# Optimization experiments

Hardware: AMD Instinct MI355X
Metric: run time of the kernel (lower is better)

## Reference

```python
import jax, jax.numpy as jnp
import numpy as np

DIM = 48
HEADS = 8
DIM1 = DIM * HEADS  # 384
RED = 16


def setup_inputs() -> dict:
    key = jax.random.key(0)
    ks = jax.random.split(key, 10)
    s = 0.02
    return {
        "x": jax.random.normal(ks[0], (4, DIM, 128, 128), dtype=jnp.float32),
        "qkv_w": jax.random.normal(ks[1], (DIM1 * 4, DIM), dtype=jnp.float32) * s,
        "dw_w": jax.random.normal(ks[2], (DIM1 * 4, HEADS, 3, 3), dtype=jnp.float32) * s,  # groups=DIM*4 -> 8 in-ch per group
        "po1_w": jax.random.normal(ks[3], (DIM, DIM1), dtype=jnp.float32) * s,
        "fc1_w": jax.random.normal(ks[4], (DIM1 // RED, DIM1), dtype=jnp.float32) * s,
        "fc1_b": jnp.zeros((DIM1 // RED,), dtype=jnp.float32),
        "fc2_w": jax.random.normal(ks[5], (DIM1, DIM1 // RED), dtype=jnp.float32) * s,
        "fc2_b": jnp.zeros((DIM1,), dtype=jnp.float32),
        "temperature": jnp.ones((HEADS, 1, 1), dtype=jnp.float32),
    }


def reference(x, qkv_w, dw_w, po1_w, fc1_w, fc1_b, fc2_w, fc2_b, temperature):
    b, c, h, w = x.shape  # c == dim
    heads = temperature.shape[0]
    # 1x1 pointwise conv: dim -> dim1*4
    qkv = jnp.einsum('bchw,oc->bohw', x, qkv_w)
    # grouped 3x3 conv, groups = dim*4 (8 channels per group)
    qkv = jax.lax.conv_general_dilated(
        qkv, dw_w, window_strides=(1, 1), padding='SAME',
        feature_group_count=c * 4,
        dimension_numbers=('NCHW', 'OIHW', 'NCHW'))
    q, k, v, l = jnp.split(qkv, 4, axis=1)  # each (b, dim1, h, w)
    hw = h * w
    q = q.reshape(b, heads, c, hw)
    k = k.reshape(b, heads, c, hw)
    v = v.reshape(b, heads, c, hw)
    # ChannelAttention on l: note it returns fc2_out * sigmoid(fc2_out)
    avg = jnp.mean(l, axis=(2, 3))  # (b, dim1)
    y = jax.nn.relu(avg @ fc1_w.T + fc1_b)
    y = y @ fc2_w.T + fc2_b  # (b, dim1)
    L = (y * jax.nn.sigmoid(y))[:, :, None, None]  # (b, dim1, 1, 1)
    # L2-normalize over spatial (last) axis, torch eps=1e-12
    q = q / jnp.clip(jnp.linalg.norm(q, axis=-1, keepdims=True), 1e-12)
    k = k / jnp.clip(jnp.linalg.norm(k, axis=-1, keepdims=True), 1e-12)
    # channel-wise attention: (b, heads, c, c)
    attn = jnp.einsum('bhcn,bhdn->bhcd', q, k) * temperature
    attn = jax.nn.softmax(attn, axis=-1)
    out = jnp.einsum('bhcd,bhdn->bhcn', attn, v).reshape(b, heads * c, h, w)
    out = L + out
    out = jnp.einsum('bchw,oc->bohw', out, po1_w) + x
    return out
```

## Files before the change

kernel.cpp:

```cpp
#include <hip/hip_runtime.h>
#include <cstdint>

#define BB 4
#define CC 48
#define HW 16384
#define D1 384
#define HEADS 8

typedef unsigned short ushort_t;
typedef __attribute__((ext_vector_type(8))) short short8;
typedef __attribute__((ext_vector_type(4))) float f32x4;

__device__ __forceinline__ float bf2f(ushort_t u){
  union{uint32_t i; float f;} v; v.i = ((uint32_t)u)<<16; return v.f;
}
__device__ __forceinline__ ushort_t f2bf(float f){
  union{float f; uint32_t i;} v; v.f=f;
  uint32_t x = v.i;
  uint32_t r = (x + 0x7fff + ((x>>16)&1)) >> 16;
  return (ushort_t)r;
}

__global__ __launch_bounds__(256) void k_wf(const float* __restrict__ dw,
                                            const float* __restrict__ qw,
                                            ushort_t* __restrict__ wfp,
                                            float* __restrict__ qn2){
  int oc = blockIdx.x, tid = threadIdx.x;
  if(oc < 19){ int i = oc*256 + tid; if(i < 4800) qn2[i] = 0.f; }
  for(int kk=tid; kk<448; kk+=256){
    int t = kk/48, c = kk - t*48;
    float s = 0.f;
    if(t < 9){
      #pragma unroll
      for(int j=0;j<8;j++)
        s += dw[(size_t)oc*72 + j*9 + t] * qw[(size_t)((oc>>3)*8 + j)*48 + c];
    }
    wfp[(size_t)oc*448 + kk] = f2bf(s);
  }
}

__global__ __launch_bounds__(256) void k_xpose(const float* __restrict__ x,
                                               ushort_t* __restrict__ xb16,
                                               float* __restrict__ xst){
  int gy = blockIdx.x;
  int b  = blockIdx.y;
  ushort_t* orow = xb16 + ((size_t)b*130 + gy)*130*48;
  int tid = threadIdx.x;
  if(gy==0 || gy==129){
    short8 z = {0,0,0,0,0,0,0,0};
    for(int u=tid; u<780; u+=256) *(short8*)(orow + u*8) = z;
    return;
  }
  __shared__ float xl[48*128];
  const float* xr = x + (size_t)b*CC*HW + (size_t)(gy-1)*128;
  for(int i=tid;i<6144;i+=256){
    int c=i>>7, p=i&127;
    xl[c*128+p] = xr[(size_t)c*HW + p];
  }
  __syncthreads();
  for(int u=tid; u<780; u+=256){
    int gx = u/6, s = u-gx*6;
    ushort_t tmp[8];
    if(gx==0||gx==129){
      #pragma unroll
      for(int j=0;j<8;j++) tmp[j]=0;
    } else {
      #pragma unroll
      for(int j=0;j<8;j++) tmp[j] = f2bf(xl[(s*8+j)*128 + (gx-1)]);
    }
    *(short8*)(orow + (size_t)u*8) = *(short8*)tmp;
  }
  if(tid < 48){
    const float* row = &xl[tid*128];
    float a0=0,a1=0,a2=0,a3=0;
    #pragma unroll 8
    for(int p=0;p<128;p+=4){ a0+=row[p]; a1+=row[p+1]; a2+=row[p+2]; a3+=row[p+3]; }
    float s = (a0+a1)+(a2+a3);
    float* o = xst + ((size_t)b*48 + tid)*9;
    atomicAdd(&o[0], s);
    atomicAdd(&o[3], row[0]);
    atomicAdd(&o[4], row[127]);
    if(gy==1)  { o[1]=s; o[5]=row[0]; o[6]=row[127]; }
    if(gy==128){ o[2]=s; o[7]=row[0]; o[8]=row[127]; }
  }
}

#define HROWC 64
__global__ __launch_bounds__(256,3) void k_conv(const ushort_t* __restrict__ xb16,
                                                const ushort_t* __restrict__ wfp,
                                                ushort_t* __restrict__ qkvd){
  __shared__ __align__(16) ushort_t xs[180*HROWC];
  int tid  = threadIdx.x;
  int wave = tid>>6, lane = tid&63;
  int quad = lane>>4, mrow = lane&15;
  int mhalf = wave>>1, nhalf = wave&1;
  int tile = blockIdx.x;
  int ty0 = (tile>>3)*8, tx0 = (tile&7)*16;
  int ocb = blockIdx.y*128 + mhalf*64;
  int b   = blockIdx.z;

  const ushort_t* xh = xb16 + ((size_t)b*16900 + (size_t)ty0*130 + tx0)*48;
  for(int u=tid; u<1944; u+=256){
    int r = u/6, g = u - r*6;
    int hy = r/18, hx = r - hy*18;
    short8 v = *(const short8*)(xh + ((size_t)hy*130 + hx)*48 + g*8);
    *(short8*)(xs + r*HROWC + ((g ^ (r&7))<<3)) = v;
  }
  __syncthreads();

  int rb[4];
  #pragma unroll
  for(int nt=0;nt<4;nt++) rb[nt] = (nhalf*4+nt+1)*18 + mrow + 1;

  const ushort_t* Abase = wfp + (size_t)(ocb + mrow)*448 + quad*8;
  f32x4 Cacc[4][4];
  #pragma unroll
  for(int mt=0;mt<4;mt++)
    #pragma unroll
    for(int nt=0;nt<4;nt++) Cacc[mt][nt] = (f32x4){0.f,0.f,0.f,0.f};

  short8 Ac[4], An[4];
  #pragma unroll
  for(int mt=0;mt<4;mt++) Ac[mt] = *(const short8*)(Abase + (size_t)mt*16*448);

  #pragma unroll
  for(int chunk=0; chunk<14; chunk++){
    if(chunk < 13){
      #pragma unroll
      for(int mt=0;mt<4;mt++)
        An[mt] = *(const short8*)(Abase + (size_t)mt*16*448 + (chunk+1)*32);
    }
    int kq = chunk*32 + quad*8;
    int t  = kq/48;
    int c  = kq - t*48;
    int tc = (t<9) ? t : 8;
    int dyq = tc/3;
    int drow = dyq*18 + (tc - dyq*3) - 19;
    int g = c>>3;
    short8 Bf[4];
    #pragma unroll
    for(int nt=0;nt<4;nt++){
      int r = rb[nt] + drow;
      Bf[nt] = *(const short8*)(xs + r*HROWC + ((g ^ (r&7))<<3));
    }
    #pragma unroll
    for(int mt=0;mt<4;mt++)
      #pragma unroll
      for(int nt=0;nt<4;nt++)
        Cacc[mt][nt] = __builtin_amdgcn_mfma_f32_16x16x32_bf16(Ac[mt], Bf[nt], Cacc[mt][nt], 0,0,0);
    #pragma unroll
    for(int mt=0;mt<4;mt++) Ac[mt] = An[mt];
  }

  #pragma unroll
  for(int mt=0;mt<4;mt++){
    #pragma unroll
    for(int nt=0;nt<4;nt++){
      int py = nhalf*4 + nt;
      int gpos = (ty0+py)*128 + tx0 + mrow;
      #pragma unroll
      for(int r=0;r<4;r++){
        int oc = ocb + mt*16 + quad*4 + r;
        qkvd[((size_t)b*1152 + oc)*HW + gpos] = f2bf(Cacc[mt][nt][r]);
      }
    }
  }
}

__global__ __launch_bounds__(256,3) void k_S(const ushort_t* __restrict__ qkvd,
                                             float* __restrict__ Spart,
                                             float* __restrict__ qn2){
  __shared__ __align__(16) ushort_t qk[96*264];
  int tid = threadIdx.x;
  int blk = blockIdx.x, h = blockIdx.y, b = blockIdx.z;
  int wave = tid>>6, lane = tid&63;
  int quad = lane>>4, mrow = lane&15;
  const ushort_t* qb = qkvd + ((size_t)b*1152 + h*48)*HW;
  const ushort_t* kb = qb + (size_t)384*HW;

  f32x4 accS[3][3], accq[3], acck[3];
  #pragma unroll
  for(int mt=0;mt<3;mt++){
    accq[mt] = (f32x4){0.f,0.f,0.f,0.f};
    acck[mt] = (f32x4){0.f,0.f,0.f,0.f};
    #pragma unroll
    for(int nt=0;nt<3;nt++) accS[mt][nt] = (f32x4){0.f,0.f,0.f,0.f};
  }

  for(int half=0; half<2; half++){
    int p0 = blk*512 + half*256;
    __syncthreads();
    for(int u=tid; u<3072; u+=256){
      int ch = u>>5, px = u&31;
      const ushort_t* src = ((ch<48) ? qb + (size_t)ch*HW
                                     : kb + (size_t)(ch-48)*HW) + p0 + px*8;
      *(short8*)(qk + ch*264 + px*8) = *(const short8*)src;
    }
    __syncthreads();
    #pragma unroll
    for(int ks=0; ks<2; ks++){
      int koff = wave*64 + ks*32 + quad*8;
      short8 Aq[3], Bk[3];
      #pragma unroll
      for(int mt=0;mt<3;mt++) Aq[mt] = *(const short8*)(qk + (mt*16+mrow)*264 + koff);
      #pragma unroll
      for(int nt=0;nt<3;nt++) Bk[nt] = *(const short8*)(qk + (48+nt*16+mrow)*264 + koff);
      #pragma unroll
      for(int mt=0;mt<3;mt++){
        accq[mt] = __builtin_amdgcn_mfma_f32_16x16x32_bf16(Aq[mt], Aq[mt], accq[mt], 0,0,0);
        acck[mt] = __builtin_amdgcn_mfma_f32_16x16x32_bf16(Bk[mt], Bk[mt], acck[mt], 0,0,0);
        #pragma unroll
        for(int nt=0;nt<3;nt++)
          accS[mt][nt] = __builtin_amdgcn_mfma_f32_16x16x32_bf16(Aq[mt], Bk[nt], accS[mt][nt], 0,0,0);
      }
    }
  }
  __syncthreads();
  float* scr = (float*)qk;
  #pragma unroll
  for(int mt=0;mt<3;mt++)
    #pragma unroll
    for(int nt=0;nt<3;nt++)
      #pragma unroll
      for(int r=0;r<4;r++)
        scr[wave*2304 + (mt*16+quad*4+r)*48 + nt*16 + mrow] = accS[mt][nt][r];
  __syncthreads();
  float* outp = Spart + ((size_t)((b*HEADS+h)*32 + blk))*2304;
  for(int idx=tid; idx<2304; idx+=256)
    outp[idx] = scr[idx] + scr[2304+idx] + scr[4608+idx] + scr[6912+idx];
  int rr = mrow - (quad<<2);
  #pragma unroll
  for(int r=0;r<4;r++){
    if(rr == r){
      #pragma unroll
      for(int mt=0;mt<3;mt++){
        atomicAdd(qn2 + (size_t)b*D1 + h*48 + mt*16 + mrow, accq[mt][r]);
        atomicAdd(qn2 + 1536 + (size_t)b*D1 + h*48 + mt*16 + mrow, acck[mt][r]);
      }
    }
  }
}

__global__ __launch_bounds__(384) void k_mlp(const float* __restrict__ xst,
                                             const float* __restrict__ qw,
                                             const float* __restrict__ dw,
                                             const float* __restrict__ fc1w,
                                             const float* __restrict__ fc1b,
                                             const float* __restrict__ fc2w,
                                             const float* __restrict__ fc2b,
                                             const float* __restrict__ po1,
                                             float* __restrict__ constv){
  int b = blockIdx.x, tid = threadIdx.x;
  __shared__ float xsl[432];
  __shared__ float lst[3456];
  __shared__ float avg[384];
  __shared__ float y1[24];
  __shared__ float Lb[384];
  for(int i=tid;i<432;i+=384) xsl[i] = xst[(size_t)b*432 + i];
  __syncthreads();
  {
    float st[9];
    #pragma unroll
    for(int s=0;s<9;s++) st[s]=0.f;
    const float* w = qw + (size_t)(1152+tid)*48;
    for(int c=0;c<48;c++){
      float wv = w[c];
      #pragma unroll
      for(int s=0;s<9;s++) st[s] += wv*xsl[c*9+s];
    }
    #pragma unroll
    for(int s=0;s<9;s++) lst[tid*9+s] = st[s];
  }
  __syncthreads();
  {
    int base = tid & ~7;
    const float* ls = &lst[base*9];
    float s = 0.f;
    #pragma unroll
    for(int i=0;i<8;i++){
      float T=ls[i*9+0],R0=ls[i*9+1],R1=ls[i*9+2],C0=ls[i*9+3],C1=ls[i*9+4];
      float c00=ls[i*9+5],c0W=ls[i*9+6],cH0=ls[i*9+7],cHW=ls[i*9+8];
      const float* wp = dw + (size_t)(1152+tid)*72 + i*9;
      #pragma unroll
      for(int dy=0;dy<3;dy++){
        float rm = (dy==0)?R1:((dy==2)?R0:0.f);
        #pragma unroll
        for(int dx=0;dx<3;dx++){
          float cm = (dx==0)?C1:((dx==2)?C0:0.f);
          float corner = 0.f;
          if(dy==0&&dx==0)corner=cHW;
          if(dy==0&&dx==2)corner=cH0;
          if(dy==2&&dx==0)corner=c0W;
          if(dy==2&&dx==2)corner=c00;
          s += wp[dy*3+dx]*(T-rm-cm+corner);
        }
      }
    }
    avg[tid] = s*(1.f/16384.f);
  }
  __syncthreads();
  if(tid<24){
    float s = fc1b[tid];
    const float* w = fc1w + (size_t)tid*384;
    for(int c=0;c<384;c++) s += w[c]*avg[c];
    y1[tid] = fmaxf(s,0.f);
  }
  __syncthreads();
  {
    float s = fc2b[tid];
    const float* w = fc2w + (size_t)tid*24;
    #pragma unroll
    for(int j=0;j<24;j++) s += w[j]*y1[j];
    Lb[tid] = s/(1.f+__expf(-s));
  }
  __syncthreads();
  if(tid<48){
    const float* w = po1 + (size_t)tid*384;
    float s = 0.f;
    for(int c=0;c<384;c++) s += w[c]*Lb[c];
    constv[b*48+tid] = s;
  }
}

__global__ __launch_bounds__(256) void k_attn(const float* __restrict__ Spart,
                                              const float* __restrict__ qn2,
                                              const float* __restrict__ temp,
                                              const float* __restrict__ po1,
                                              ushort_t* __restrict__ m2o){
  int h = blockIdx.x, b = blockIdx.y, tid = threadIdx.x;
  __shared__ float att[2304];
  __shared__ float nq[48], nk[48];
  const float* kn2 = qn2 + 1536;
  if(tid<48)      nq[tid]    = fmaxf(sqrtf(qn2[(size_t)b*D1 + h*48 + tid]),    1e-12f);
  else if(tid<96) nk[tid-48] = fmaxf(sqrtf(kn2[(size_t)b*D1 + h*48 + tid-48]), 1e-12f);
  __syncthreads();
  float tmp = temp[h];
  const float* Sp = Spart + ((size_t)(b*HEADS+h)*32)*2304;
  for(int idx=tid; idx<2304; idx+=256){
    float s = 0.f;
    for(int blk=0;blk<32;blk++) s += Sp[(size_t)blk*2304 + idx];
    int c = idx/48, d = idx - c*48;
    att[idx] = s*tmp/(nq[c]*nk[d]);
  }
  __syncthreads();
  if(tid<48){
    float* row = &att[tid*48];
    float m = -1e30f;
    for(int d=0;d<48;d++) m = fmaxf(m,row[d]);
    float s = 0.f;
    for(int d=0;d<48;d++){ float e=__expf(row[d]-m); row[d]=e; s+=e; }
    float inv = 1.f/s;
    for(int d=0;d<48;d++) row[d]*=inv;
  }
  __syncthreads();
  for(int idx=tid; idx<2304; idx+=256){
    int d = idx/48, o = idx - d*48;
    float s = 0.f;
    for(int c=0;c<48;c++) s += po1[(size_t)o*D1 + h*48 + c]*att[c*48+d];
    m2o[((size_t)b*48 + o)*D1 + h*48 + d] = f2bf(s);
  }
}

#define FROW2 40
__global__ __launch_bounds__(256,3) void k_final(const ushort_t* __restrict__ qkvd,
                                                 const ushort_t* __restrict__ m2o,
                                                 const float* __restrict__ constv,
                                                 const float* __restrict__ x,
                                                 float* __restrict__ out){
  __shared__ __align__(16) ushort_t vT[2][128*FROW2];
  int tid = threadIdx.x;
  int wave = tid>>6, lane = tid&63;
  int quad = lane>>4, mrow = lane&15;
  int pos0 = blockIdx.x*128;
  int b = blockIdx.y;
  const ushort_t* vb = qkvd + ((size_t)b*1152 + 768)*HW + pos0;
  const ushort_t* Ab = m2o + (size_t)b*48*D1;
  f32x4 acc[3][2];
  #pragma unroll
  for(int mt=0;mt<3;mt++)
    #pragma unroll
    for(int nt=0;nt<2;nt++) acc[mt][nt] = (f32x4){0.f,0.f,0.f,0.f};

  auto stage = [&](int ck, int buf){
    #pragma unroll
    for(int s=0;s<2;s++){
      int unit = tid + s*256;
      int ch = unit>>4, pg = unit&15, p0 = pg*8;
      int chg = ch>>3, cl = ch&7;
      short8 v = *(const short8*)(vb + (size_t)(ck*32+ch)*HW + p0);
      ushort_t tmp[8]; *(short8*)tmp = v;
      #pragma unroll
      for(int i=0;i<8;i++){
        int p = p0+i;
        int sl = (chg ^ (p&3) ^ ((p>>3)&3)) & 3;
        vT[buf][p*FROW2 + (sl<<3) + cl] = tmp[i];
      }
    }
  };
  stage(0,0);
  __syncthreads();
  for(int ck=0; ck<12; ck++){
    if(ck<11) stage(ck+1, (ck+1)&1);
    short8 Af[3], Bf[2];
    #pragma unroll
    for(int mt=0;mt<3;mt++)
      Af[mt] = *(const short8*)(Ab + (size_t)(mt*16+mrow)*D1 + ck*32 + quad*8);
    #pragma unroll
    for(int nt=0;nt<2;nt++){
      int p = wave*32 + nt*16 + mrow;
      int sl = (quad ^ (p&3) ^ ((p>>3)&3)) & 3;
      Bf[nt] = *(const short8*)(&vT[ck&1][p*FROW2 + (sl<<3)]);
    }
    #pragma unroll
    for(int mt=0;mt<3;mt++)
      #pragma unroll
      for(int nt=0;nt<2;nt++)
        acc[mt][nt] = __builtin_amdgcn_mfma_f32_16x16x32_bf16(Af[mt], Bf[nt], acc[mt][nt], 0,0,0);
    __syncthreads();
  }
  const float* xb = x + (size_t)b*CC*HW + pos0;
  float* ob = out + (size_t)b*CC*HW + pos0;
  #pragma unroll
  for(int mt=0;mt<3;mt++)
    #pragma unroll
    for(int nt=0;nt<2;nt++){
      int p = wave*32 + nt*16 + mrow;
      #pragma unroll
      for(int r=0;r<4;r++){
        int o = mt*16 + quad*4 + r;
        ob[(size_t)o*HW + p] = xb[(size_t)o*HW + p] + constv[b*48+o] + acc[mt][nt][r];
      }
    }
}

extern "C" void kernel_launch(void* const* d_in, const int* in_sizes, int n_in,
                              void* d_out, int out_size, void* d_ws, size_t ws_size,
                              hipStream_t stream){
  const float* x    = (const float*)d_in[0];
  const float* qw   = (const float*)d_in[1];
  const float* dw   = (const float*)d_in[2];
  const float* po1  = (const float*)d_in[3];
  const float* fc1w = (const float*)d_in[4];
  const float* fc1b = (const float*)d_in[5];
  const float* fc2w = (const float*)d_in[6];
  const float* fc2b = (const float*)d_in[7];
  const float* temp = (const float*)d_in[8];
  float* out = (float*)d_out;
  char* ws = (char*)d_ws;

  ushort_t* qkvd   = (ushort_t*)(ws);
  float*    Spart  = (float*)(ws + 150994944);
  ushort_t* xb16   = (ushort_t*)(ws + 150994944);
  float*    qn2    = (float*)(ws + 160432128);
  float*    xst    = (float*)(ws + 160444416);
  float*    constv = (float*)(ws + 160451328);
  ushort_t* m2o    = (ushort_t*)(ws + 160452096);
  ushort_t* wfp    = (ushort_t*)(ws + 160599552);

  k_wf    <<<dim3(1152),         256, 0, stream>>>(dw, qw, wfp, qn2);
  k_xpose <<<dim3(130,BB),       256, 0, stream>>>(x, xb16, xst);
  k_conv  <<<dim3(128,9,BB),     256, 0, stream>>>(xb16, wfp, qkvd);
  k_S     <<<dim3(32,HEADS,BB),  256, 0, stream>>>(qkvd, Spart, qn2);
  k_mlp   <<<dim3(BB),           384, 0, stream>>>(xst, qw, dw, fc1w, fc1b, fc2w, fc2b, po1, constv);
  k_attn  <<<dim3(HEADS,BB),     256, 0, stream>>>(Spart, qn2, temp, po1, m2o);
  k_final <<<dim3(128,BB),       256, 0, stream>>>(qkvd, m2o, constv, x, out);
}
```

Measured before the change: 343.2 us.

## Coalesce conv output stores via LDS staging and atomically reduce S partials

The conv kernel epilogue now stages bf16 results in shared memory and writes 16-byte vectors contiguous along spatial positions, replacing scattered 2-byte stores. The S kernel now accumulates its per-block Gram partials directly into a single zero-initialized buffer with float atomics, removing the 32-way partial buffer and the reduction loop in the attention kernel. The zeroing is folded into the weight-prep kernel. This adds extra barriers in the conv epilogue and introduces atomic contention and nondeterministic summation order.

```diff
diff --git a/kernel.cpp b/kernel.cpp
--- a/kernel.cpp
+++ b/kernel.cpp
@@ -24,9 +24,11 @@
 __global__ __launch_bounds__(256) void k_wf(const float* __restrict__ dw,
                                             const float* __restrict__ qw,
                                             ushort_t* __restrict__ wfp,
-                                            float* __restrict__ qn2){
+                                            float* __restrict__ qn2,
+                                            float* __restrict__ sred){
   int oc = blockIdx.x, tid = threadIdx.x;
   if(oc < 19){ int i = oc*256 + tid; if(i < 4800) qn2[i] = 0.f; }
+  if(oc >= 32 && oc < 320){ sred[(oc-32)*256 + tid] = 0.f; }
   for(int kk=tid; kk<448; kk+=256){
     int t = kk/48, c = kk - t*48;
     float s = 0.f;
@@ -96,7 +98,8 @@
   int mhalf = wave>>1, nhalf = wave&1;
   int tile = blockIdx.x;
   int ty0 = (tile>>3)*8, tx0 = (tile&7)*16;
-  int ocb = blockIdx.y*128 + mhalf*64;
+  int ocb0 = blockIdx.y*128;
+  int ocb  = ocb0 + mhalf*64;
   int b   = blockIdx.z;
 
   const ushort_t* xh = xb16 + ((size_t)b*16900 + (size_t)ty0*130 + tx0)*48;
@@ -152,23 +155,38 @@
     for(int mt=0;mt<4;mt++) Ac[mt] = An[mt];
   }
 
-  #pragma unroll
-  for(int mt=0;mt<4;mt++){
-    #pragma unroll
-    for(int nt=0;nt<4;nt++){
-      int py = nhalf*4 + nt;
-      int gpos = (ty0+py)*128 + tx0 + mrow;
-      #pragma unroll
-      for(int r=0;r<4;r++){
-        int oc = ocb + mt*16 + quad*4 + r;
-        qkvd[((size_t)b*1152 + oc)*HW + gpos] = f2bf(Cacc[mt][nt][r]);
-      }
+  ushort_t* ld = xs;
+  #pragma unroll
+  for(int p=0;p<2;p++){
+    __syncthreads();
+    #pragma unroll
+    for(int m2=0;m2<2;m2++){
+      int mt = p*2 + m2;
+      int lo = mhalf*32 + m2*16 + quad*4;
+      #pragma unroll
+      for(int nt=0;nt<4;nt++){
+        int pos = (nhalf*4+nt)*16 + mrow;
+        #pragma unroll
+        for(int r=0;r<4;r++)
+          ld[(lo+r)*132 + pos] = f2bf(Cacc[mt][nt][r]);
+      }
+    }
+    __syncthreads();
+    #pragma unroll
+    for(int k=0;k<4;k++){
+      int u = tid + k*256;
+      int ol = u>>4, sub = u&15;
+      int py = sub>>1, half = sub&1;
+      short8 v = *(const short8*)(ld + ol*132 + py*16 + half*8);
+      int oc128 = (ol>>5)*64 + p*32 + (ol&31);
+      int gpos = (ty0+py)*128 + tx0 + half*8;
+      *(short8*)(qkvd + ((size_t)b*1152 + ocb0 + oc128)*HW + gpos) = v;
     }
   }
 }
 
 __global__ __launch_bounds__(256,3) void k_S(const ushort_t* __restrict__ qkvd,
-                                             float* __restrict__ Spart,
+                                             float* __restrict__ sred,
                                              float* __restrict__ qn2){
   __shared__ __align__(16) ushort_t qk[96*264];
   int tid = threadIdx.x;
@@ -215,19 +233,14 @@
       }
     }
   }
-  __syncthreads();
-  float* scr = (float*)qk;
+  float* outp = sred + (size_t)(b*HEADS+h)*2304;
   #pragma unroll
   for(int mt=0;mt<3;mt++)
     #pragma unroll
     for(int nt=0;nt<3;nt++)
       #pragma unroll
       for(int r=0;r<4;r++)
-        scr[wave*2304 + (mt*16+quad*4+r)*48 + nt*16 + mrow] = accS[mt][nt][r];
-  __syncthreads();
-  float* outp = Spart + ((size_t)((b*HEADS+h)*32 + blk))*2304;
-  for(int idx=tid; idx<2304; idx+=256)
-    outp[idx] = scr[idx] + scr[2304+idx] + scr[4608+idx] + scr[6912+idx];
+        atomicAdd(&outp[(mt*16+quad*4+r)*48 + nt*16 + mrow], accS[mt][nt][r]);
   int rr = mrow - (quad<<2);
   #pragma unroll
   for(int r=0;r<4;r++){
@@ -322,7 +335,7 @@
   }
 }
 
-__global__ __launch_bounds__(256) void k_attn(const float* __restrict__ Spart,
+__global__ __launch_bounds__(256) void k_attn(const float* __restrict__ sred,
                                               const float* __restrict__ qn2,
                                               const float* __restrict__ temp,
                                               const float* __restrict__ po1,
@@ -335,12 +348,10 @@
   else if(tid<96) nk[tid-48] = fmaxf(sqrtf(kn2[(size_t)b*D1 + h*48 + tid-48]), 1e-12f);
   __syncthreads();
   float tmp = temp[h];
-  const float* Sp = Spart + ((size_t)(b*HEADS+h)*32)*2304;
+  const float* Sp = sred + (size_t)(b*HEADS+h)*2304;
   for(int idx=tid; idx<2304; idx+=256){
-    float s = 0.f;
-    for(int blk=0;blk<32;blk++) s += Sp[(size_t)blk*2304 + idx];
     int c = idx/48, d = idx - c*48;
-    att[idx] = s*tmp/(nq[c]*nk[d]);
+    att[idx] = Sp[idx]*tmp/(nq[c]*nk[d]);
   }
   __syncthreads();
   if(tid<48){
@@ -449,19 +460,19 @@
   char* ws = (char*)d_ws;
 
   ushort_t* qkvd   = (ushort_t*)(ws);
-  float*    Spart  = (float*)(ws + 150994944);
   ushort_t* xb16   = (ushort_t*)(ws + 150994944);
   float*    qn2    = (float*)(ws + 160432128);
   float*    xst    = (float*)(ws + 160444416);
   float*    constv = (float*)(ws + 160451328);
   ushort_t* m2o    = (ushort_t*)(ws + 160452096);
   ushort_t* wfp    = (ushort_t*)(ws + 160599552);
-
-  k_wf    <<<dim3(1152),         256, 0, stream>>>(dw, qw, wfp, qn2);
+  float*    sred   = (float*)(ws + 161631744);
+
+  k_wf    <<<dim3(1152),         256, 0, stream>>>(dw, qw, wfp, qn2, sred);
   k_xpose <<<dim3(130,BB),       256, 0, stream>>>(x, xb16, xst);
   k_conv  <<<dim3(128,9,BB),     256, 0, stream>>>(xb16, wfp, qkvd);
-  k_S     <<<dim3(32,HEADS,BB),  256, 0, stream>>>(qkvd, Spart, qn2);
+  k_S     <<<dim3(32,HEADS,BB),  256, 0, stream>>>(qkvd, sred, qn2);
   k_mlp   <<<dim3(BB),           384, 0, stream>>>(xst, qw, dw, fc1w, fc1b, fc2w, fc2b, po1, constv);
-  k_attn  <<<dim3(HEADS,BB),     256, 0, stream>>>(Spart, qn2, temp, po1, m2o);
+  k_attn  <<<dim3(HEADS,BB),     256, 0, stream>>>(sred, qn2, temp, po1, m2o);
   k_final <<<dim3(128,BB),       256, 0, stream>>>(qkvd, m2o, constv, x, out);
 }
```

New measurement: 381.7 us. 1.11x slower.
